# Performance work log

Hardware: AMD Instinct MI355X
Metric: run time of the kernel (lower is better)

The kernel has to match this reference:

```python
import jax, jax.numpy as jnp
import numpy as np

N_NODES = 100000
N_EDGES = 3200000
D_IN = 96      # sum(latent_dim)
D_OUT = 32     # latent_dim[-1]
N_HEADS = 4
LEAKY_SLOPE = 0.2


def setup_inputs() -> dict:
    key = jax.random.key(0)
    k_x, k_w, k_a, k_src, k_dst = jax.random.split(key, 5)
    x = jax.random.normal(k_x, (N_NODES, D_IN), dtype=jnp.float32)
    # per-head GAT params (xavier-ish scale)
    W = jax.random.normal(k_w, (N_HEADS, D_IN, D_OUT), dtype=jnp.float32) * (1.414 / np.sqrt(D_IN))
    a = jax.random.normal(k_a, (N_HEADS, 2 * D_OUT), dtype=jnp.float32) * 0.1
    edge_src = jax.random.randint(k_src, (N_EDGES,), 0, N_NODES)
    edge_dst = jax.random.randint(k_dst, (N_EDGES,), 0, N_NODES)
    return {"x": x, "W": W, "a": a, "edge_src": edge_src, "edge_dst": edge_dst}


def reference(x, W, a, edge_src, edge_dst):
    # Multi-head sparse GAT layer (SpGraphAttentionLayer, concat=True, eval mode).
    N = x.shape[0]
    n_heads, _, d_out = W.shape
    outs = []
    for i in range(n_heads):  # small fixed head loop; data dims fully vectorized
        h = x @ W[i]                                   # [N, d_out]
        # a @ cat(h[src], h[dst]) == h[src]@a1 + h[dst]@a2 (avoids [E, 2*d_out] concat)
        s = h[edge_src] @ a[i, :d_out] + h[edge_dst] @ a[i, d_out:]   # [E]
        edge_e = jnp.exp(-jax.nn.leaky_relu(s, LEAKY_SLOPE))          # [E]
        # sparse_coo(edge, edge_e, [N,N]) @ h  ==  scatter-add of edge_e * h[dst] into src
        msg = edge_e[:, None] * h[edge_dst]                           # [E, d_out]
        h_prime = jax.ops.segment_sum(msg, edge_src, num_segments=N)  # [N, d_out]
        outs.append(jax.nn.elu(h_prime))
    return jnp.concatenate(outs, axis=1)  # [N, n_heads * d_out]
```

## Files before the change

kernel.cpp:

```cpp
#include <hip/hip_runtime.h>
#include <hip/hip_bf16.h>

#define DIN 96
#define DOUT 32
#define NH 4
#define DTOT 128
#define SLOPE 0.2f
#define NPB 16
#define BSH 7
#define BNODES 128
#define MAXB 1024
#define EPB 16384

__device__ __forceinline__ unsigned int packbf2(float lo, float hi) {
    unsigned int a = __float_as_uint(lo), b = __float_as_uint(hi);
    a += 0x7fffu + ((a >> 16) & 1u);
    b += 0x7fffu + ((b >> 16) & 1u);
    return (a >> 16) | (b & 0xffff0000u);
}

__global__ __launch_bounds__(256) void feat_kernel(
    const float* __restrict__ x, const float* __restrict__ W,
    const float* __restrict__ a,
    unsigned int* __restrict__ hq,
    float2* __restrict__ usrc, float2* __restrict__ vdst,
    int n_nodes)
{
    __shared__ float Wl[DIN * DTOT];
    __shared__ float xs[NPB * DIN];
    __shared__ float al[NH * 2 * DOUT];
    const int t = threadIdx.x;

    for (int i = t; i < DIN * DTOT; i += 256) {
        int k = i >> 7, c = i & 127;
        int head = c >> 5, j = c & 31;
        Wl[i] = W[head * (DIN * DOUT) + k * DOUT + j];
    }
    for (int i = t; i < NH * 2 * DOUT; i += 256) al[i] = a[i];

    const int node0 = blockIdx.x * NPB;
    for (int i = t; i < NPB * DIN; i += 256) {
        int gidx = node0 * DIN + i;
        xs[i] = (gidx < n_nodes * DIN) ? x[gidx] : 0.f;
    }
    __syncthreads();

    const int node = t >> 4;
    const int cb = (t & 15) << 3;
    float acc[8];
#pragma unroll
    for (int j = 0; j < 8; ++j) acc[j] = 0.f;

#pragma unroll 4
    for (int k = 0; k < DIN; ++k) {
        float xv = xs[node * DIN + k];
#pragma unroll
        for (int j = 0; j < 8; ++j)
            acc[j] += xv * Wl[k * DTOT + cb + j];
    }

    const int g = node0 + node;
    if (g < n_nodes) {
        uint4 pk;
        pk.x = packbf2(acc[0], acc[1]);
        pk.y = packbf2(acc[2], acc[3]);
        pk.z = packbf2(acc[4], acc[5]);
        pk.w = packbf2(acc[6], acc[7]);
        *(uint4*)&hq[(size_t)g * 64 + (cb >> 1)] = pk;
    }

    const int head = cb >> 5;
    const int j0 = cb & 31;
    float ps = 0.f, pd = 0.f;
#pragma unroll
    for (int j = 0; j < 8; ++j) {
        ps += acc[j] * al[head * 64 + j0 + j];
        pd += acc[j] * al[head * 64 + 32 + j0 + j];
    }
    ps += __shfl_xor(ps, 1); ps += __shfl_xor(ps, 2);
    pd += __shfl_xor(pd, 1); pd += __shfl_xor(pd, 2);
    if ((t & 3) == 0 && g < n_nodes) {
        usrc[g * NH + head] = make_float2(__expf(-ps), __expf(-SLOPE * ps));
        vdst[g * NH + head] = make_float2(__expf(-pd), __expf(-SLOPE * pd));
    }
}


__global__ __launch_bounds__(256) void bincount_kernel(
    const int* __restrict__ esrc, int* __restrict__ counts, int n_edges, int nb)
{
    __shared__ int bc[MAXB];
    const int t = threadIdx.x;
    for (int i = t; i < nb; i += 256) bc[i] = 0;
    __syncthreads();
    const int base = blockIdx.x * EPB;
    const int end = min(base + EPB, n_edges);
    for (int e = base + t; e < end; e += 256)
        atomicAdd(&bc[esrc[e] >> BSH], 1);
    __syncthreads();
    for (int i = t; i < nb; i += 256)
        if (bc[i] > 0) atomicAdd(&counts[i], bc[i]);
}

__global__ __launch_bounds__(1024) void bscan_kernel(
    const int* __restrict__ counts, int* __restrict__ bbase,
    int* __restrict__ gcur, int* __restrict__ sbase, int nb)
{
    __shared__ int tmp[1024];
    const int t = threadIdx.x;
    int v = (t < nb) ? counts[t] : 0;
    tmp[t] = v;
    __syncthreads();
    for (int off = 1; off < 1024; off <<= 1) {
        int xv = (t >= off) ? tmp[t - off] : 0;
        __syncthreads();
        tmp[t] += xv;
        __syncthreads();
    }
    if (t < nb) {
        int excl = tmp[t] - v;
        bbase[t] = excl;
        gcur[t] = excl;
        sbase[t] = ((excl + 3) & ~3) + t * (4 * BNODES);
    }
}

__global__ __launch_bounds__(256) void binscatter_kernel(
    const int* __restrict__ esrc, const int* __restrict__ edst,
    int* __restrict__ gcur, unsigned int* __restrict__ binned,
    int n_edges, int nb)
{
    __shared__ int bc[MAXB];
    const int t = threadIdx.x;
    for (int i = t; i < nb; i += 256) bc[i] = 0;
    __syncthreads();
    const int base = blockIdx.x * EPB;
    const int end = min(base + EPB, n_edges);
    for (int e = base + t; e < end; e += 256)
        atomicAdd(&bc[esrc[e] >> BSH], 1);
    __syncthreads();
    for (int i = t; i < nb; i += 256) {
        int c = bc[i];
        bc[i] = (c > 0) ? atomicAdd(&gcur[i], c) : 0;
    }
    __syncthreads();
    for (int e = base + t; e < end; e += 256) {
        int s = esrc[e];
        int pos = atomicAdd(&bc[s >> BSH], 1);
        binned[pos] = ((unsigned int)(s & (BNODES - 1)) << 17) | (unsigned int)edst[e];
    }
}

__global__ __launch_bounds__(256) void binfine_kernel(
    const unsigned int* __restrict__ binned,
    const int* __restrict__ counts, const int* __restrict__ bbase,
    const int* __restrict__ sbase,
    int* __restrict__ offs, int* __restrict__ deg,
    int* __restrict__ slots, int n_nodes)
{
    __shared__ int dcnt[BNODES];
    __shared__ int sc[BNODES];
    __shared__ int dcur[BNODES];
    const int t = threadIdx.x;
    const int b = blockIdx.x;
    const int cnt = counts[b];
    const int start = bbase[b];
    const int sb = sbase[b];
    const int node0 = b << BSH;

    if (t < BNODES) dcnt[t] = 0;
    __syncthreads();
    for (int i = t; i < cnt; i += 256)
        atomicAdd(&dcnt[binned[start + i] >> 17], 1);
    __syncthreads();
    int pd = 0;
    if (t < BNODES) { pd = (dcnt[t] + 3) & ~3; sc[t] = pd; }
    __syncthreads();
    for (int off = 1; off < BNODES; off <<= 1) {
        int v = 0;
        if (t < BNODES && t >= off) v = sc[t - off];
        __syncthreads();
        if (t < BNODES) sc[t] += v;
        __syncthreads();
    }
    if (t < BNODES) {
        int o = sb + sc[t] - pd;
        dcur[t] = o;
        int node = node0 + t;
        if (node < n_nodes) { offs[node] = o; deg[node] = dcnt[t]; }
    }
    __syncthreads();
    for (int i = t; i < cnt; i += 256) {
        unsigned int w = binned[start + i];
        int pos = atomicAdd(&dcur[w >> 17], 1);
        slots[pos] = (int)(w & 0x1ffffu);
    }
}

__global__ __launch_bounds__(256) void gather_kernel(
    const int* __restrict__ slots, const int* __restrict__ offsets,
    const int* __restrict__ deg,
    const unsigned int* __restrict__ hv,
    const float2* __restrict__ usrc, const float2* __restrict__ vdst,
    float* __restrict__ out, int n_nodes)
{
    const int t = threadIdx.x;
    const int node = blockIdx.x * 4 + (t >> 6);
    if (node >= n_nodes) return;
    const int l = t & 63;
    const int head = l >> 4;
    const float2 u = usrc[node * NH + head];
    const int beg = offsets[node];
    const int d = deg[node];

    float ax0 = 0.f, ay0 = 0.f, ax1 = 0.f, ay1 = 0.f;
    float ax2 = 0.f, ay2 = 0.f, ax3 = 0.f, ay3 = 0.f;
    int k = 0;
    int4 dd = (d >= 4) ? *(const int4*)(slots + beg) : make_int4(0, 0, 0, 0);
    for (; k + 4 <= d; k += 4) {
        const int4 cur = dd;
        if (k + 8 <= d) dd = *(const int4*)(slots + beg + k + 4);
        float2 v0 = vdst[cur.x * NH + head];
        float2 v1 = vdst[cur.y * NH + head];
        float2 v2 = vdst[cur.z * NH + head];
        float2 v3 = vdst[cur.w * NH + head];
        unsigned int w0 = hv[(size_t)cur.x * 64 + l];
        unsigned int w1 = hv[(size_t)cur.y * 64 + l];
        unsigned int w2 = hv[(size_t)cur.z * 64 + l];
        unsigned int w3 = hv[(size_t)cur.w * 64 + l];
        float e0 = fminf(u.x * v0.x, u.y * v0.y);
        float e1 = fminf(u.x * v1.x, u.y * v1.y);
        float e2 = fminf(u.x * v2.x, u.y * v2.y);
        float e3 = fminf(u.x * v3.x, u.y * v3.y);
        ax0 = fmaf(e0, __uint_as_float(w0 << 16), ax0);
        ay0 = fmaf(e0, __uint_as_float(w0 & 0xffff0000u), ay0);
        ax1 = fmaf(e1, __uint_as_float(w1 << 16), ax1);
        ay1 = fmaf(e1, __uint_as_float(w1 & 0xffff0000u), ay1);
        ax2 = fmaf(e2, __uint_as_float(w2 << 16), ax2);
        ay2 = fmaf(e2, __uint_as_float(w2 & 0xffff0000u), ay2);
        ax3 = fmaf(e3, __uint_as_float(w3 << 16), ax3);
        ay3 = fmaf(e3, __uint_as_float(w3 & 0xffff0000u), ay3);
    }
    for (; k < d; ++k) {
        int dst = slots[beg + k];
        float2 v = vdst[dst * NH + head];
        unsigned int w = hv[(size_t)dst * 64 + l];
        float e = fminf(u.x * v.x, u.y * v.y);
        ax0 = fmaf(e, __uint_as_float(w << 16), ax0);
        ay0 = fmaf(e, __uint_as_float(w & 0xffff0000u), ay0);
    }
    float rx = (ax0 + ax1) + (ax2 + ax3);
    float ry = (ay0 + ay1) + (ay2 + ay3);
    rx = rx > 0.f ? rx : __expf(rx) - 1.f;
    ry = ry > 0.f ? ry : __expf(ry) - 1.f;
    ((float2*)out)[(size_t)node * 64 + l] = make_float2(rx, ry);
}

extern "C" void kernel_launch(void* const* d_in, const int* in_sizes, int n_in,
                              void* d_out, int out_size, void* d_ws, size_t ws_size,
                              hipStream_t stream)
{
    const float* x  = (const float*)d_in[0];
    const float* W  = (const float*)d_in[1];
    const float* a  = (const float*)d_in[2];
    const int* esrc = (const int*)d_in[3];
    const int* edst = (const int*)d_in[4];
    const int n_nodes = in_sizes[0] / DIN;
    const int n_edges = in_sizes[3];
    float* out = (float*)d_out;

    const int nb = (n_nodes + BNODES - 1) >> BSH;

    unsigned int* hq = (unsigned int*)d_ws;
    float2* usrc = (float2*)(hq + (size_t)n_nodes * 64);
    float2* vdst = usrc + (size_t)n_nodes * NH;
    int* offs   = (int*)(vdst + (size_t)n_nodes * NH);
    int* deg    = offs + n_nodes;
    int* counts = deg + n_nodes;
    int* bbase  = counts + MAXB;
    int* gcur   = bbase + MAXB;
    int* sbase  = gcur + MAXB;
    unsigned int* binned = (unsigned int*)(sbase + MAXB);
    int* slots  = (int*)(binned + n_edges);

    hipMemsetAsync(counts, 0, MAXB * sizeof(int), stream);

    feat_kernel<<<(n_nodes + NPB - 1) / NPB, 256, 0, stream>>>(
        x, W, a, hq, usrc, vdst, n_nodes);

    const int binblocks = (n_edges + EPB - 1) / EPB;
    bincount_kernel<<<binblocks, 256, 0, stream>>>(esrc, counts, n_edges, nb);
    bscan_kernel<<<1, 1024, 0, stream>>>(counts, bbase, gcur, sbase, nb);
    binscatter_kernel<<<binblocks, 256, 0, stream>>>(
        esrc, edst, gcur, binned, n_edges, nb);
    binfine_kernel<<<nb, 256, 0, stream>>>(
        binned, counts, bbase, sbase, offs, deg, slots, n_nodes);

    gather_kernel<<<(n_nodes + 3) / 4, 256, 0, stream>>>(
        slots, offs, deg, hq, usrc, vdst, out, n_nodes);
}
```

Baseline: 499.5 us.

## Vectorize binning loads, pad global bin counters, and unroll gather by eight

The binning kernels now read source and destination indices as int4 and process four edges per thread iteration. Edges per block drop from 16384 to 4096. Global bin counters and cursors are padded to 16 ints apart to reduce atomic contention on shared cache lines. Per-bin bases are aligned to 4 so binfine can use uint4 loads, and the gather loop is unrolled to 8 neighbours to expose more memory-level parallelism, at the cost of more registers and a larger scalar tail for low-degree nodes.

```diff
diff --git a/kernel.cpp b/kernel.cpp
--- a/kernel.cpp
+++ b/kernel.cpp
@@ -10,7 +10,8 @@
 #define BSH 7
 #define BNODES 128
 #define MAXB 1024
-#define EPB 16384
+#define EPB 4096
+#define CPAD 16
 
 __device__ __forceinline__ unsigned int packbf2(float lo, float hi) {
     unsigned int a = __float_as_uint(lo), b = __float_as_uint(hi);
@@ -95,11 +96,18 @@
     __syncthreads();
     const int base = blockIdx.x * EPB;
     const int end = min(base + EPB, n_edges);
-    for (int e = base + t; e < end; e += 256)
-        atomicAdd(&bc[esrc[e] >> BSH], 1);
-    __syncthreads();
-    for (int i = t; i < nb; i += 256)
-        if (bc[i] > 0) atomicAdd(&counts[i], bc[i]);
+    int i = base + (t << 2);
+    for (; i + 3 < end; i += 1024) {
+        int4 s4 = *(const int4*)(esrc + i);
+        atomicAdd(&bc[s4.x >> BSH], 1);
+        atomicAdd(&bc[s4.y >> BSH], 1);
+        atomicAdd(&bc[s4.z >> BSH], 1);
+        atomicAdd(&bc[s4.w >> BSH], 1);
+    }
+    for (; i < end; ++i) atomicAdd(&bc[esrc[i] >> BSH], 1);
+    __syncthreads();
+    for (int k = t; k < nb; k += 256)
+        if (bc[k] > 0) atomicAdd(&counts[k * CPAD], bc[k]);
 }
 
 __global__ __launch_bounds__(1024) void bscan_kernel(
@@ -108,7 +116,7 @@
 {
     __shared__ int tmp[1024];
     const int t = threadIdx.x;
-    int v = (t < nb) ? counts[t] : 0;
+    int v = (t < nb) ? counts[t * CPAD] : 0;
     tmp[t] = v;
     __syncthreads();
     for (int off = 1; off < 1024; off <<= 1) {
@@ -119,8 +127,9 @@
     }
     if (t < nb) {
         int excl = tmp[t] - v;
-        bbase[t] = excl;
-        gcur[t] = excl;
+        int ab = ((excl + 3) & ~3) + t * 4;
+        bbase[t] = ab;
+        gcur[t * CPAD] = ab;
         sbase[t] = ((excl + 3) & ~3) + t * (4 * BNODES);
     }
 }
@@ -136,18 +145,38 @@
     __syncthreads();
     const int base = blockIdx.x * EPB;
     const int end = min(base + EPB, n_edges);
-    for (int e = base + t; e < end; e += 256)
-        atomicAdd(&bc[esrc[e] >> BSH], 1);
-    __syncthreads();
-    for (int i = t; i < nb; i += 256) {
-        int c = bc[i];
-        bc[i] = (c > 0) ? atomicAdd(&gcur[i], c) : 0;
-    }
-    __syncthreads();
-    for (int e = base + t; e < end; e += 256) {
-        int s = esrc[e];
+    int i = base + (t << 2);
+    for (; i + 3 < end; i += 1024) {
+        int4 s4 = *(const int4*)(esrc + i);
+        atomicAdd(&bc[s4.x >> BSH], 1);
+        atomicAdd(&bc[s4.y >> BSH], 1);
+        atomicAdd(&bc[s4.z >> BSH], 1);
+        atomicAdd(&bc[s4.w >> BSH], 1);
+    }
+    for (; i < end; ++i) atomicAdd(&bc[esrc[i] >> BSH], 1);
+    __syncthreads();
+    for (int k = t; k < nb; k += 256) {
+        int c = bc[k];
+        bc[k] = (c > 0) ? atomicAdd(&gcur[k * CPAD], c) : 0;
+    }
+    __syncthreads();
+    i = base + (t << 2);
+    for (; i + 3 < end; i += 1024) {
+        int4 s4 = *(const int4*)(esrc + i);
+        int4 d4 = *(const int4*)(edst + i);
+        int p0 = atomicAdd(&bc[s4.x >> BSH], 1);
+        int p1 = atomicAdd(&bc[s4.y >> BSH], 1);
+        int p2 = atomicAdd(&bc[s4.z >> BSH], 1);
+        int p3 = atomicAdd(&bc[s4.w >> BSH], 1);
+        binned[p0] = ((unsigned int)(s4.x & (BNODES - 1)) << 17) | (unsigned int)d4.x;
+        binned[p1] = ((unsigned int)(s4.y & (BNODES - 1)) << 17) | (unsigned int)d4.y;
+        binned[p2] = ((unsigned int)(s4.z & (BNODES - 1)) << 17) | (unsigned int)d4.z;
+        binned[p3] = ((unsigned int)(s4.w & (BNODES - 1)) << 17) | (unsigned int)d4.w;
+    }
+    for (; i < end; ++i) {
+        int s = esrc[i];
         int pos = atomicAdd(&bc[s >> BSH], 1);
-        binned[pos] = ((unsigned int)(s & (BNODES - 1)) << 17) | (unsigned int)edst[e];
+        binned[pos] = ((unsigned int)(s & (BNODES - 1)) << 17) | (unsigned int)edst[i];
     }
 }
 
@@ -163,15 +192,22 @@
     __shared__ int dcur[BNODES];
     const int t = threadIdx.x;
     const int b = blockIdx.x;
-    const int cnt = counts[b];
+    const int cnt = counts[b * CPAD];
     const int start = bbase[b];
     const int sb = sbase[b];
     const int node0 = b << BSH;
 
     if (t < BNODES) dcnt[t] = 0;
     __syncthreads();
-    for (int i = t; i < cnt; i += 256)
-        atomicAdd(&dcnt[binned[start + i] >> 17], 1);
+    int i = t << 2;
+    for (; i + 3 < cnt; i += 1024) {
+        uint4 w4 = *(const uint4*)(binned + start + i);
+        atomicAdd(&dcnt[w4.x >> 17], 1);
+        atomicAdd(&dcnt[w4.y >> 17], 1);
+        atomicAdd(&dcnt[w4.z >> 17], 1);
+        atomicAdd(&dcnt[w4.w >> 17], 1);
+    }
+    for (; i < cnt; ++i) atomicAdd(&dcnt[binned[start + i] >> 17], 1);
     __syncthreads();
     int pd = 0;
     if (t < BNODES) { pd = (dcnt[t] + 3) & ~3; sc[t] = pd; }
@@ -190,7 +226,19 @@
         if (node < n_nodes) { offs[node] = o; deg[node] = dcnt[t]; }
     }
     __syncthreads();
-    for (int i = t; i < cnt; i += 256) {
+    i = t << 2;
+    for (; i + 3 < cnt; i += 1024) {
+        uint4 w4 = *(const uint4*)(binned + start + i);
+        int p0 = atomicAdd(&dcur[w4.x >> 17], 1);
+        int p1 = atomicAdd(&dcur[w4.y >> 17], 1);
+        int p2 = atomicAdd(&dcur[w4.z >> 17], 1);
+        int p3 = atomicAdd(&dcur[w4.w >> 17], 1);
+        slots[p0] = (int)(w4.x & 0x1ffffu);
+        slots[p1] = (int)(w4.y & 0x1ffffu);
+        slots[p2] = (int)(w4.z & 0x1ffffu);
+        slots[p3] = (int)(w4.w & 0x1ffffu);
+    }
+    for (; i < cnt; ++i) {
         unsigned int w = binned[start + i];
         int pos = atomicAdd(&dcur[w >> 17], 1);
         slots[pos] = (int)(w & 0x1ffffu);
@@ -216,22 +264,41 @@
     float ax0 = 0.f, ay0 = 0.f, ax1 = 0.f, ay1 = 0.f;
     float ax2 = 0.f, ay2 = 0.f, ax3 = 0.f, ay3 = 0.f;
     int k = 0;
-    int4 dd = (d >= 4) ? *(const int4*)(slots + beg) : make_int4(0, 0, 0, 0);
-    for (; k + 4 <= d; k += 4) {
-        const int4 cur = dd;
-        if (k + 8 <= d) dd = *(const int4*)(slots + beg + k + 4);
-        float2 v0 = vdst[cur.x * NH + head];
-        float2 v1 = vdst[cur.y * NH + head];
-        float2 v2 = vdst[cur.z * NH + head];
-        float2 v3 = vdst[cur.w * NH + head];
-        unsigned int w0 = hv[(size_t)cur.x * 64 + l];
-        unsigned int w1 = hv[(size_t)cur.y * 64 + l];
-        unsigned int w2 = hv[(size_t)cur.z * 64 + l];
-        unsigned int w3 = hv[(size_t)cur.w * 64 + l];
+    int4 d0, d1;
+    if (d >= 8) {
+        d0 = *(const int4*)(slots + beg);
+        d1 = *(const int4*)(slots + beg + 4);
+    }
+    for (; k + 8 <= d; k += 8) {
+        const int4 c0 = d0, c1 = d1;
+        if (k + 16 <= d) {
+            d0 = *(const int4*)(slots + beg + k + 8);
+            d1 = *(const int4*)(slots + beg + k + 12);
+        }
+        float2 v0 = vdst[c0.x * NH + head];
+        float2 v1 = vdst[c0.y * NH + head];
+        float2 v2 = vdst[c0.z * NH + head];
+        float2 v3 = vdst[c0.w * NH + head];
+        float2 v4 = vdst[c1.x * NH + head];
+        float2 v5 = vdst[c1.y * NH + head];
+        float2 v6 = vdst[c1.z * NH + head];
+        float2 v7 = vdst[c1.w * NH + head];
+        unsigned int w0 = hv[(size_t)c0.x * 64 + l];
+        unsigned int w1 = hv[(size_t)c0.y * 64 + l];
+        unsigned int w2 = hv[(size_t)c0.z * 64 + l];
+        unsigned int w3 = hv[(size_t)c0.w * 64 + l];
+        unsigned int w4 = hv[(size_t)c1.x * 64 + l];
+        unsigned int w5 = hv[(size_t)c1.y * 64 + l];
+        unsigned int w6 = hv[(size_t)c1.z * 64 + l];
+        unsigned int w7 = hv[(size_t)c1.w * 64 + l];
         float e0 = fminf(u.x * v0.x, u.y * v0.y);
         float e1 = fminf(u.x * v1.x, u.y * v1.y);
         float e2 = fminf(u.x * v2.x, u.y * v2.y);
         float e3 = fminf(u.x * v3.x, u.y * v3.y);
+        float e4 = fminf(u.x * v4.x, u.y * v4.y);
+        float e5 = fminf(u.x * v5.x, u.y * v5.y);
+        float e6 = fminf(u.x * v6.x, u.y * v6.y);
+        float e7 = fminf(u.x * v7.x, u.y * v7.y);
         ax0 = fmaf(e0, __uint_as_float(w0 << 16), ax0);
         ay0 = fmaf(e0, __uint_as_float(w0 & 0xffff0000u), ay0);
         ax1 = fmaf(e1, __uint_as_float(w1 << 16), ax1);
@@ -240,6 +307,14 @@
         ay2 = fmaf(e2, __uint_as_float(w2 & 0xffff0000u), ay2);
         ax3 = fmaf(e3, __uint_as_float(w3 << 16), ax3);
         ay3 = fmaf(e3, __uint_as_float(w3 & 0xffff0000u), ay3);
+        ax0 = fmaf(e4, __uint_as_float(w4 << 16), ax0);
+        ay0 = fmaf(e4, __uint_as_float(w4 & 0xffff0000u), ay0);
+        ax1 = fmaf(e5, __uint_as_float(w5 << 16), ax1);
+        ay1 = fmaf(e5, __uint_as_float(w5 & 0xffff0000u), ay1);
+        ax2 = fmaf(e6, __uint_as_float(w6 << 16), ax2);
+        ay2 = fmaf(e6, __uint_as_float(w6 & 0xffff0000u), ay2);
+        ax3 = fmaf(e7, __uint_as_float(w7 << 16), ax3);
+        ay3 = fmaf(e7, __uint_as_float(w7 & 0xffff0000u), ay3);
     }
     for (; k < d; ++k) {
         int dst = slots[beg + k];
@@ -277,13 +352,13 @@
     int* offs   = (int*)(vdst + (size_t)n_nodes * NH);
     int* deg    = offs + n_nodes;
     int* counts = deg + n_nodes;
-    int* bbase  = counts + MAXB;
-    int* gcur   = bbase + MAXB;
-    int* sbase  = gcur + MAXB;
+    int* gcur   = counts + MAXB * CPAD;
+    int* bbase  = gcur + MAXB * CPAD;
+    int* sbase  = bbase + MAXB;
     unsigned int* binned = (unsigned int*)(sbase + MAXB);
-    int* slots  = (int*)(binned + n_edges);
-
-    hipMemsetAsync(counts, 0, MAXB * sizeof(int), stream);
+    int* slots  = (int*)(binned + n_edges + 4 * MAXB + 64);
+
+    hipMemsetAsync(counts, 0, MAXB * CPAD * sizeof(int), stream);
 
     feat_kernel<<<(n_nodes + NPB - 1) / NPB, 256, 0, stream>>>(
         x, W, a, hq, usrc, vdst, n_nodes);
```

Result: slower. 510.4 us (+2.2%).

## Replace global atomic bin cursors with per-block count matrix and two-level scan

Applied to the files above, without the earlier changes.

The binning pass now stores per-block histograms into a count matrix instead of atomically accumulating global counts. A second scan kernel computes each block's write offset per bin, so the scatter pass no longer recounts edges or hits global atomics. Edge loads in count, scatter and fine-bin kernels are vectorized to int4/uint4, and EPB is halved to create more blocks. Bin starts are padded to 16-byte alignment for the vector loads. The cost is an extra kernel launch, a larger workspace and a serial loop over blocks in scanB.

```diff
diff --git a/kernel.cpp b/kernel.cpp
--- a/kernel.cpp
+++ b/kernel.cpp
@@ -10,7 +10,8 @@
 #define BSH 7
 #define BNODES 128
 #define MAXB 1024
-#define EPB 16384
+#define EPB 8192
+#define BMAX 512
 
 __device__ __forceinline__ unsigned int packbf2(float lo, float hi) {
     unsigned int a = __float_as_uint(lo), b = __float_as_uint(hi);
@@ -87,7 +88,8 @@
 
 
 __global__ __launch_bounds__(256) void bincount_kernel(
-    const int* __restrict__ esrc, int* __restrict__ counts, int n_edges, int nb)
+    const int* __restrict__ esrc, int* __restrict__ counts,
+    int n_edges, int nb)
 {
     __shared__ int bc[MAXB];
     const int t = threadIdx.x;
@@ -95,21 +97,31 @@
     __syncthreads();
     const int base = blockIdx.x * EPB;
     const int end = min(base + EPB, n_edges);
-    for (int e = base + t; e < end; e += 256)
-        atomicAdd(&bc[esrc[e] >> BSH], 1);
-    __syncthreads();
-    for (int i = t; i < nb; i += 256)
-        if (bc[i] > 0) atomicAdd(&counts[i], bc[i]);
-}
-
-__global__ __launch_bounds__(1024) void bscan_kernel(
-    const int* __restrict__ counts, int* __restrict__ bbase,
-    int* __restrict__ gcur, int* __restrict__ sbase, int nb)
+    int i = base + (t << 2);
+    for (; i + 3 < end; i += 1024) {
+        int4 s4 = *(const int4*)(esrc + i);
+        atomicAdd(&bc[s4.x >> BSH], 1);
+        atomicAdd(&bc[s4.y >> BSH], 1);
+        atomicAdd(&bc[s4.z >> BSH], 1);
+        atomicAdd(&bc[s4.w >> BSH], 1);
+    }
+    for (; i < end; ++i) atomicAdd(&bc[esrc[i] >> BSH], 1);
+    __syncthreads();
+    for (int k = t; k < nb; k += 256)
+        counts[blockIdx.x * nb + k] = bc[k];
+}
+
+__global__ __launch_bounds__(1024) void scanB_kernel(
+    const int* __restrict__ counts, int* __restrict__ Tk,
+    int* __restrict__ bbase, int* __restrict__ sbase, int nb, int B)
 {
     __shared__ int tmp[1024];
     const int t = threadIdx.x;
-    int v = (t < nb) ? counts[t] : 0;
-    tmp[t] = v;
+    int s = 0;
+    if (t < nb) {
+        for (int b = 0; b < B; ++b) s += counts[b * nb + t];
+    }
+    tmp[t] = s;
     __syncthreads();
     for (int off = 1; off < 1024; off <<= 1) {
         int xv = (t >= off) ? tmp[t - off] : 0;
@@ -118,42 +130,67 @@
         __syncthreads();
     }
     if (t < nb) {
-        int excl = tmp[t] - v;
-        bbase[t] = excl;
-        gcur[t] = excl;
+        int excl = tmp[t] - s;
+        Tk[t] = s;
+        bbase[t] = ((excl + 3) & ~3) + t * 4;
         sbase[t] = ((excl + 3) & ~3) + t * (4 * BNODES);
     }
+}
+
+__global__ __launch_bounds__(512) void scanC_kernel(
+    const int* __restrict__ counts, const int* __restrict__ bbase,
+    int* __restrict__ woff, int nb, int B)
+{
+    __shared__ int tmp[512];
+    const int k = blockIdx.x;
+    const int t = threadIdx.x;
+    int v = (t < B) ? counts[t * nb + k] : 0;
+    tmp[t] = v;
+    __syncthreads();
+    for (int off = 1; off < 512; off <<= 1) {
+        int xv = (t >= off) ? tmp[t - off] : 0;
+        __syncthreads();
+        tmp[t] += xv;
+        __syncthreads();
+    }
+    if (t < B) woff[k * B + t] = bbase[k] + tmp[t] - v;
 }
 
 __global__ __launch_bounds__(256) void binscatter_kernel(
     const int* __restrict__ esrc, const int* __restrict__ edst,
-    int* __restrict__ gcur, unsigned int* __restrict__ binned,
-    int n_edges, int nb)
-{
-    __shared__ int bc[MAXB];
-    const int t = threadIdx.x;
-    for (int i = t; i < nb; i += 256) bc[i] = 0;
-    __syncthreads();
-    const int base = blockIdx.x * EPB;
+    const int* __restrict__ woff, unsigned int* __restrict__ binned,
+    int n_edges, int nb, int B)
+{
+    __shared__ int cur[MAXB];
+    const int t = threadIdx.x;
+    const int b = blockIdx.x;
+    for (int k = t; k < nb; k += 256) cur[k] = woff[k * B + b];
+    __syncthreads();
+    const int base = b * EPB;
     const int end = min(base + EPB, n_edges);
-    for (int e = base + t; e < end; e += 256)
-        atomicAdd(&bc[esrc[e] >> BSH], 1);
-    __syncthreads();
-    for (int i = t; i < nb; i += 256) {
-        int c = bc[i];
-        bc[i] = (c > 0) ? atomicAdd(&gcur[i], c) : 0;
-    }
-    __syncthreads();
-    for (int e = base + t; e < end; e += 256) {
-        int s = esrc[e];
-        int pos = atomicAdd(&bc[s >> BSH], 1);
-        binned[pos] = ((unsigned int)(s & (BNODES - 1)) << 17) | (unsigned int)edst[e];
+    int i = base + (t << 2);
+    for (; i + 3 < end; i += 1024) {
+        int4 s4 = *(const int4*)(esrc + i);
+        int4 d4 = *(const int4*)(edst + i);
+        int p0 = atomicAdd(&cur[s4.x >> BSH], 1);
+        int p1 = atomicAdd(&cur[s4.y >> BSH], 1);
+        int p2 = atomicAdd(&cur[s4.z >> BSH], 1);
+        int p3 = atomicAdd(&cur[s4.w >> BSH], 1);
+        binned[p0] = ((unsigned int)(s4.x & (BNODES - 1)) << 17) | (unsigned int)d4.x;
+        binned[p1] = ((unsigned int)(s4.y & (BNODES - 1)) << 17) | (unsigned int)d4.y;
+        binned[p2] = ((unsigned int)(s4.z & (BNODES - 1)) << 17) | (unsigned int)d4.z;
+        binned[p3] = ((unsigned int)(s4.w & (BNODES - 1)) << 17) | (unsigned int)d4.w;
+    }
+    for (; i < end; ++i) {
+        int s = esrc[i];
+        int pos = atomicAdd(&cur[s >> BSH], 1);
+        binned[pos] = ((unsigned int)(s & (BNODES - 1)) << 17) | (unsigned int)edst[i];
     }
 }
 
 __global__ __launch_bounds__(256) void binfine_kernel(
     const unsigned int* __restrict__ binned,
-    const int* __restrict__ counts, const int* __restrict__ bbase,
+    const int* __restrict__ Tk, const int* __restrict__ bbase,
     const int* __restrict__ sbase,
     int* __restrict__ offs, int* __restrict__ deg,
     int* __restrict__ slots, int n_nodes)
@@ -163,15 +200,22 @@
     __shared__ int dcur[BNODES];
     const int t = threadIdx.x;
     const int b = blockIdx.x;
-    const int cnt = counts[b];
+    const int cnt = Tk[b];
     const int start = bbase[b];
     const int sb = sbase[b];
     const int node0 = b << BSH;
 
     if (t < BNODES) dcnt[t] = 0;
     __syncthreads();
-    for (int i = t; i < cnt; i += 256)
-        atomicAdd(&dcnt[binned[start + i] >> 17], 1);
+    int i = t << 2;
+    for (; i + 3 < cnt; i += 1024) {
+        uint4 w4 = *(const uint4*)(binned + start + i);
+        atomicAdd(&dcnt[w4.x >> 17], 1);
+        atomicAdd(&dcnt[w4.y >> 17], 1);
+        atomicAdd(&dcnt[w4.z >> 17], 1);
+        atomicAdd(&dcnt[w4.w >> 17], 1);
+    }
+    for (; i < cnt; ++i) atomicAdd(&dcnt[binned[start + i] >> 17], 1);
     __syncthreads();
     int pd = 0;
     if (t < BNODES) { pd = (dcnt[t] + 3) & ~3; sc[t] = pd; }
@@ -190,7 +234,19 @@
         if (node < n_nodes) { offs[node] = o; deg[node] = dcnt[t]; }
     }
     __syncthreads();
-    for (int i = t; i < cnt; i += 256) {
+    i = t << 2;
+    for (; i + 3 < cnt; i += 1024) {
+        uint4 w4 = *(const uint4*)(binned + start + i);
+        int p0 = atomicAdd(&dcur[w4.x >> 17], 1);
+        int p1 = atomicAdd(&dcur[w4.y >> 17], 1);
+        int p2 = atomicAdd(&dcur[w4.z >> 17], 1);
+        int p3 = atomicAdd(&dcur[w4.w >> 17], 1);
+        slots[p0] = (int)(w4.x & 0x1ffffu);
+        slots[p1] = (int)(w4.y & 0x1ffffu);
+        slots[p2] = (int)(w4.z & 0x1ffffu);
+        slots[p3] = (int)(w4.w & 0x1ffffu);
+    }
+    for (; i < cnt; ++i) {
         unsigned int w = binned[start + i];
         int pos = atomicAdd(&dcur[w >> 17], 1);
         slots[pos] = (int)(w & 0x1ffffu);
@@ -270,31 +326,32 @@
     float* out = (float*)d_out;
 
     const int nb = (n_nodes + BNODES - 1) >> BSH;
+    const int B  = (n_edges + EPB - 1) / EPB;
+    const int nbB = ((nb * B + 3) & ~3);
 
     unsigned int* hq = (unsigned int*)d_ws;
     float2* usrc = (float2*)(hq + (size_t)n_nodes * 64);
     float2* vdst = usrc + (size_t)n_nodes * NH;
     int* offs   = (int*)(vdst + (size_t)n_nodes * NH);
     int* deg    = offs + n_nodes;
-    int* counts = deg + n_nodes;
-    int* bbase  = counts + MAXB;
-    int* gcur   = bbase + MAXB;
-    int* sbase  = gcur + MAXB;
-    unsigned int* binned = (unsigned int*)(sbase + MAXB);
-    int* slots  = (int*)(binned + n_edges);
-
-    hipMemsetAsync(counts, 0, MAXB * sizeof(int), stream);
+    int* Tk     = deg + n_nodes;
+    int* bbase  = Tk + MAXB;
+    int* sbase  = bbase + MAXB;
+    int* counts = sbase + MAXB;
+    int* woff   = counts + nbB;
+    unsigned int* binned = (unsigned int*)(woff + nbB);
+    int* slots  = (int*)(binned + n_edges + 4 * nb + 64);
 
     feat_kernel<<<(n_nodes + NPB - 1) / NPB, 256, 0, stream>>>(
         x, W, a, hq, usrc, vdst, n_nodes);
 
-    const int binblocks = (n_edges + EPB - 1) / EPB;
-    bincount_kernel<<<binblocks, 256, 0, stream>>>(esrc, counts, n_edges, nb);
-    bscan_kernel<<<1, 1024, 0, stream>>>(counts, bbase, gcur, sbase, nb);
-    binscatter_kernel<<<binblocks, 256, 0, stream>>>(
-        esrc, edst, gcur, binned, n_edges, nb);
+    bincount_kernel<<<B, 256, 0, stream>>>(esrc, counts, n_edges, nb);
+    scanB_kernel<<<1, 1024, 0, stream>>>(counts, Tk, bbase, sbase, nb, B);
+    scanC_kernel<<<nb, 512, 0, stream>>>(counts, bbase, woff, nb, B);
+    binscatter_kernel<<<B, 256, 0, stream>>>(
+        esrc, edst, woff, binned, n_edges, nb, B);
     binfine_kernel<<<nb, 256, 0, stream>>>(
-        binned, counts, bbase, sbase, offs, deg, slots, n_nodes);
+        binned, Tk, bbase, sbase, offs, deg, slots, n_nodes);
 
     gather_kernel<<<(n_nodes + 3) / 4, 256, 0, stream>>>(
         slots, offs, deg, hq, usrc, vdst, out, n_nodes);
```

Result: slower. 560.2 us (+12.2%).
